# Optimization experiments

Hardware: AMD Instinct MI355X
Metric: run time of the kernel (lower is better)

Reference implementation:

```python
import jax, jax.numpy as jnp
import numpy as np

GRID_SIZE = 5
K = 3  # spline order
WIDTH = [512, 1024, 1024, 1024, 256]
BATCH = 4096


def make_grid(in_dim):
    # pykan-style extended uniform grid on [-1, 1]: G + 2K + 1 knots per input dim
    h = 2.0 / GRID_SIZE
    pts = jnp.arange(-K, GRID_SIZE + K + 1, dtype=jnp.float32) * h - 1.0
    return jnp.tile(pts[None, :], (in_dim, 1))


def bspline_basis(x, grid):
    # Cox-de Boor recursion. x: [B, in], grid: [in, G+2K+1] -> basis [B, in, G+K]
    xe = x[..., None]
    b = ((xe >= grid[:, :-1]) & (xe < grid[:, 1:])).astype(x.dtype)  # degree 0: [B, in, G+2K]
    for d in range(1, K + 1):
        left = (xe - grid[:, :-(d + 1)]) / (grid[:, d:-1] - grid[:, :-(d + 1)]) * b[..., :-1]
        right = (grid[:, d + 1:] - xe) / (grid[:, d + 1:] - grid[:, 1:-d]) * b[..., 1:]
        b = left + right
    return b


def kan_layer(x, grid, coef, scale_base, scale_sp):
    # out_j = sum_i scale_base[i,j]*silu(x_i) + scale_sp[i,j]*sum_g coef[i,j,g]*B_g(x_i)
    basis = bspline_basis(x, grid)                                   # [B, in, G+K]
    base = jnp.einsum('bi,io->bo', jax.nn.silu(x), scale_base)
    spline = jnp.einsum('big,iog->bo', basis, coef * scale_sp[:, :, None])
    return base + spline


def setup_inputs() -> dict:
    key = jax.random.key(0)
    n_layers = len(WIDTH) - 1
    keys = jax.random.split(key, 2 + 2 * n_layers)
    inp = {
        'inputs_y': jax.random.normal(keys[0], (BATCH, 256), dtype=jnp.float32) * 0.5,
        'inputs_u': jax.random.normal(keys[1], (BATCH, 256), dtype=jnp.float32) * 0.5,
    }
    for l, (din, dout) in enumerate(zip(WIDTH[:-1], WIDTH[1:])):
        inp[f'coef{l}'] = jax.random.normal(keys[2 + 2 * l], (din, dout, GRID_SIZE + K), dtype=jnp.float32) * (0.1 / np.sqrt(din))
        inp[f'sb{l}'] = jax.random.normal(keys[3 + 2 * l], (din, dout), dtype=jnp.float32) * (1.0 / np.sqrt(din))
        inp[f'ss{l}'] = jnp.ones((din, dout), dtype=jnp.float32)
        inp[f'grid{l}'] = make_grid(din)
    return inp


def reference(inputs_y, inputs_u,
              coef0, sb0, ss0, grid0,
              coef1, sb1, ss1, grid1,
              coef2, sb2, ss2, grid2,
              coef3, sb3, ss3, grid3):
    x = jnp.concatenate([inputs_y.astype(jnp.float32), inputs_u.astype(jnp.float32)], axis=-1)
    layers = [(grid0, coef0, sb0, ss0), (grid1, coef1, sb1, ss1),
              (grid2, coef2, sb2, ss2), (grid3, coef3, sb3, ss3)]
    for g, c, sb, ss in layers:
        x = kan_layer(x, g, c, sb, ss)
    return x
```

## Files before the change

kernel.cpp:

```cpp
#include <hip/hip_runtime.h>
#include <cstdint>
#include <cstddef>

typedef _Float16 f16;
typedef _Float16 f16x2 __attribute__((ext_vector_type(2)));
typedef _Float16 f16x4 __attribute__((ext_vector_type(4)));
typedef _Float16 f16x8 __attribute__((ext_vector_type(8)));
typedef float f32x4 __attribute__((ext_vector_type(4)));

__device__ __forceinline__ void gl2lds16(const void* g, void* l) {
  __builtin_amdgcn_global_load_lds(
      (const __attribute__((address_space(1))) void*)(uintptr_t)g,
      (__attribute__((address_space(3))) void*)(uintptr_t)l,
      16, 0, 0);
}

__device__ __forceinline__ void kan_basis(float x, f16* out9) {
  float sig  = 1.0f / (1.0f + __expf(-x));
  out9[0] = (f16)(x * sig);

  float t[12];
#pragma unroll
  for (int j = 0; j < 12; ++j) t[j] = (float)(j - 3) * 0.4f - 1.0f;
  float b0[11];
#pragma unroll
  for (int j = 0; j < 11; ++j)
    b0[j] = (x >= t[j] && x < t[j + 1]) ? 1.0f : 0.0f;
  float b1[10];
#pragma unroll
  for (int j = 0; j < 10; ++j)
    b1[j] = (x - t[j]) * 2.5f * b0[j] + (t[j + 2] - x) * 2.5f * b0[j + 1];
  float b2[9];
#pragma unroll
  for (int j = 0; j < 9; ++j)
    b2[j] = (x - t[j]) * 1.25f * b1[j] + (t[j + 3] - x) * 1.25f * b1[j + 1];
#pragma unroll
  for (int j = 0; j < 8; ++j)
    out9[1 + j] = (f16)((x - t[j]) * (1.0f / 1.2f) * b2[j] +
                        (t[j + 4] - x) * (1.0f / 1.2f) * b2[j + 1]);
}

__global__ __launch_bounds__(256) void kan_prep_feat(
    const float* __restrict__ coef, const float* __restrict__ sb,
    const float* __restrict__ ss, f16* __restrict__ Wt,
    const float* __restrict__ Xa, const float* __restrict__ Xb,
    f16* __restrict__ F,
    int dout, int din, int prepBlocks, int featB, int segW, int bShift)
{
  __shared__ float s_sb[32][32];
  __shared__ float s_ss[32][32];
  __shared__ f16 s_w[32][288];
  const int t = threadIdx.x;
  const int gid = blockIdx.x;
  const int K9 = 9 * din;

  if (gid < prepBlocks) {
    const int prepBX = dout >> 5;
    const int o0 = (gid % prepBX) * 32, i0 = (gid / prepBX) * 32;

    {
      int il = t >> 3, oc = (t & 7) * 4;
      float4 vb = *(const float4*)(sb + (size_t)(i0 + il) * dout + o0 + oc);
      float4 vs = *(const float4*)(ss + (size_t)(i0 + il) * dout + o0 + oc);
      s_sb[il][oc + 0] = vb.x; s_sb[il][oc + 1] = vb.y;
      s_sb[il][oc + 2] = vb.z; s_sb[il][oc + 3] = vb.w;
      s_ss[il][oc + 0] = vs.x; s_ss[il][oc + 1] = vs.y;
      s_ss[il][oc + 2] = vs.z; s_ss[il][oc + 3] = vs.w;
    }
    __syncthreads();

#pragma unroll
    for (int j = 0; j < 8; ++j) {
      int f  = j * 256 + t;
      int il = f >> 6, c = f & 63;
      int ol = c >> 1, gh = (c & 1) * 4;
      float4 v = *(const float4*)(coef + ((size_t)(i0 + il) * dout + (o0 + ol)) * 8 + gh);
      float ssv = s_ss[il][ol];
      f16* dst = &s_w[ol][il * 9 + 1 + gh];
      dst[0] = (f16)(v.x * ssv); dst[1] = (f16)(v.y * ssv);
      dst[2] = (f16)(v.z * ssv); dst[3] = (f16)(v.w * ssv);
    }
#pragma unroll
    for (int j = 0; j < 4; ++j) {
      int e = j * 256 + t; int il = e >> 5, ol = e & 31;
      s_w[ol][il * 9] = (f16)s_sb[il][ol];
    }
    __syncthreads();

    {
      int o = t >> 3, part = t & 7;
      f16* dstRow = Wt + (size_t)(o0 + o) * K9 + i0 + part * 4;
#pragma unroll
      for (int tp = 0; tp < 9; ++tp) {
        f16x4 v;
#pragma unroll
        for (int j = 0; j < 4; ++j) v[j] = s_w[o][(part * 4 + j) * 9 + tp];
        *(f16x4*)(dstRow + (size_t)tp * din) = v;
      }
    }
    return;
  }

  int f   = gid - prepBlocks;
  int seg = (f >= featB) ? 1 : 0;
  int fi  = f - seg * featB;
  const float* X = seg ? Xb : Xa;
  const int halfW = segW >> 1;
  int idx2 = fi * 256 + t;
  int b  = idx2 >> bShift;
  int ii = idx2 & (halfW - 1);
  int i  = seg * segW + 2 * ii;

  float2 xv = *(const float2*)(X + (size_t)b * segW + 2 * ii);
  f16 s0[9], s1[9];
  kan_basis(xv.x, s0);
  kan_basis(xv.y, s1);

  f16* o = F + (size_t)b * K9 + i;
#pragma unroll
  for (int tp = 0; tp < 9; ++tp) {
    f16x2 v; v[0] = s0[tp]; v[1] = s1[tp];
    *(f16x2*)(o + (size_t)tp * din) = v;
  }
}

template <int SPLITK>
__global__ __launch_bounds__(256, 2) void kan_gemm(
    const f16* __restrict__ A, const f16* __restrict__ Bt,
    float* __restrict__ C, int N, int K)
{
  __shared__ __align__(16) f16 lds[4][8192];
  const int tid   = threadIdx.x;
  const int lane  = tid & 63;
  const int w     = tid >> 6;
  const int waveM = w >> 1, waveN = w & 1;
  const int l16   = lane & 15, quad = lane >> 4;
  const size_t mBase = (size_t)blockIdx.y * 128;
  const size_t nBase = (size_t)blockIdx.x * 128;
  const int kChunk = K / SPLITK;
  const int k0     = blockIdx.z * kChunk;
  const int kSteps = kChunk >> 5;

  const f16* gA[2]; int lA[2];
  const f16* gB[2]; int lB[2];
#pragma unroll
  for (int r = 0; r < 2; ++r) {
    int g = r * 256 + tid, row = g >> 2;
    int cs = (g & 3) ^ ((row >> 1) & 3);
    gA[r] = A + (mBase + row) * (size_t)K + k0 + cs * 8;
    gB[r] = Bt + (nBase + row) * (size_t)K + k0 + cs * 8;
    lA[r] = (r * 256 + (tid & ~63)) * 8;
    lB[r] = 4096 + lA[r];
  }

  f32x4 acc[4][4] = {};

#pragma unroll
  for (int p = 0; p < 3; ++p) {
    f16* b = lds[p];
    int kk = p * 32;
#pragma unroll
    for (int r = 0; r < 2; ++r) {
      gl2lds16(gA[r] + kk, b + lA[r]);
      gl2lds16(gB[r] + kk, b + lB[r]);
    }
  }

  for (int s = 0; s < kSteps; ++s) {
    if (s < kSteps - 2)       asm volatile("s_waitcnt vmcnt(8)" ::: "memory");
    else if (s == kSteps - 2) asm volatile("s_waitcnt vmcnt(4)" ::: "memory");
    else                      asm volatile("s_waitcnt vmcnt(0)" ::: "memory");
    __builtin_amdgcn_s_barrier();

    if (s + 3 < kSteps) {
      int kk = (s + 3) * 32;
      f16* b = lds[(s + 3) & 3];
#pragma unroll
      for (int r = 0; r < 2; ++r) {
        gl2lds16(gA[r] + kk, b + lA[r]);
        gl2lds16(gB[r] + kk, b + lB[r]);
      }
    }

    const f16* buf = lds[s & 3];
    f16x8 af[4], bf[4];
#pragma unroll
    for (int mi = 0; mi < 4; ++mi) {
      int row = waveM * 64 + mi * 16 + l16;
      af[mi] = *(const f16x8*)(buf + row * 32 + (quad ^ ((row >> 1) & 3)) * 8);
    }
#pragma unroll
    for (int ni = 0; ni < 4; ++ni) {
      int col = waveN * 64 + ni * 16 + l16;
      bf[ni] = *(const f16x8*)(buf + 4096 + col * 32 + (quad ^ ((col >> 1) & 3)) * 8);
    }
#pragma unroll
    for (int mi = 0; mi < 4; ++mi)
#pragma unroll
      for (int ni = 0; ni < 4; ++ni)
        acc[mi][ni] = __builtin_amdgcn_mfma_f32_16x16x32_f16(
            af[mi], bf[ni], acc[mi][ni], 0, 0, 0);
  }

#pragma unroll
  for (int mi = 0; mi < 4; ++mi) {
    size_t row = mBase + waveM * 64 + mi * 16 + quad * 4;
#pragma unroll
    for (int ni = 0; ni < 4; ++ni) {
      size_t col = nBase + waveN * 64 + ni * 16 + l16;
#pragma unroll
      for (int r = 0; r < 4; ++r)
        unsafeAtomicAdd(C + (row + r) * N + col, acc[mi][ni][r]);
    }
  }
}

extern "C" void kernel_launch(void* const* d_in, const int* in_sizes, int n_in,
                              void* d_out, int out_size, void* d_ws, size_t ws_size,
                              hipStream_t stream)
{
  const float* y = (const float*)d_in[0];
  const float* u = (const float*)d_in[1];
  const float* coef[4]; const float* sb[4]; const float* ss[4];
  for (int l = 0; l < 4; ++l) {
    coef[l] = (const float*)d_in[2 + 4 * l];
    sb[l]   = (const float*)d_in[3 + 4 * l];
    ss[l]   = (const float*)d_in[4 + 4 * l];
  }
  char* ws = (char*)d_ws;
  f16*   Wt   = (f16*)(ws);
  f16*   F    = (f16*)(ws + 18874368);
  float* actA = (float*)(ws + 18874368 + 75497472);
  float* actB = (float*)(ws + 18874368 + 75497472 + 16777216);
  float* out  = (float*)d_out;
  const size_t actBytes = (size_t)4096 * 1024 * 4;

  hipMemsetAsync(actA, 0, 2 * actBytes, stream);
  hipMemsetAsync(d_out, 0, (size_t)out_size * sizeof(float), stream);

  kan_prep_feat<<<512 + 4096, 256, 0, stream>>>(
      coef[0], sb[0], ss[0], Wt, y, u, F, 1024, 512, 512, 2048, 256, 7);
  kan_gemm<2><<<dim3(8, 32, 2), 256, 0, stream>>>(F, Wt, actA, 1024, 4608);

  kan_prep_feat<<<1024 + 8192, 256, 0, stream>>>(
      coef[1], sb[1], ss[1], Wt, actA, nullptr, F, 1024, 1024, 1024, 8192, 1024, 9);
  kan_gemm<2><<<dim3(8, 32, 2), 256, 0, stream>>>(F, Wt, actB, 1024, 9216);

  hipMemsetAsync(actA, 0, actBytes, stream);

  kan_prep_feat<<<1024 + 8192, 256, 0, stream>>>(
      coef[2], sb[2], ss[2], Wt, actB, nullptr, F, 1024, 1024, 1024, 8192, 1024, 9);
  kan_gemm<2><<<dim3(8, 32, 2), 256, 0, stream>>>(F, Wt, actA, 1024, 9216);

  kan_prep_feat<<<256 + 8192, 256, 0, stream>>>(
      coef[3], sb[3], ss[3], Wt, actA, nullptr, F, 256, 1024, 256, 8192, 1024, 9);
  kan_gemm<8><<<dim3(2, 32, 8), 256, 0, stream>>>(F, Wt, out, 256, 9216);
}
```

Before: 590.9 us.

## Restructure GEMM pipeline into paired-stage double buffering and drop a memset

The GEMM main loop now processes two 32-wide k-steps per iteration from one half of the 4-slot LDS ring while prefetching the next pair into the other half. This halves the number of barriers but waits for all outstanding loads (vmcnt(0)) each iteration, which reduces prefetch depth compared with the previous three-ahead pipeline. LDS fragment offsets are hoisted out of the loop. When the workspace is large enough, a third activation buffer is used so the mid-sequence memset can be merged into the initial one.

```diff
diff --git a/kernel.cpp b/kernel.cpp
--- a/kernel.cpp
+++ b/kernel.cpp
@@ -153,10 +153,19 @@
     lB[r] = 4096 + lA[r];
   }
 
+  int aOff[4], bOff[4];
+#pragma unroll
+  for (int mi = 0; mi < 4; ++mi) {
+    int row = waveM * 64 + mi * 16 + l16;
+    aOff[mi] = row * 32 + (quad ^ ((row >> 1) & 3)) * 8;
+    int col = waveN * 64 + mi * 16 + l16;
+    bOff[mi] = 4096 + col * 32 + (quad ^ ((col >> 1) & 3)) * 8;
+  }
+
   f32x4 acc[4][4] = {};
 
 #pragma unroll
-  for (int p = 0; p < 3; ++p) {
+  for (int p = 0; p < 2; ++p) {
     f16* b = lds[p];
     int kk = p * 32;
 #pragma unroll
@@ -166,40 +175,41 @@
     }
   }
 
-  for (int s = 0; s < kSteps; ++s) {
-    if (s < kSteps - 2)       asm volatile("s_waitcnt vmcnt(8)" ::: "memory");
-    else if (s == kSteps - 2) asm volatile("s_waitcnt vmcnt(4)" ::: "memory");
-    else                      asm volatile("s_waitcnt vmcnt(0)" ::: "memory");
+  const int nw = kSteps >> 1;
+  for (int wd = 0; wd < nw; ++wd) {
+    asm volatile("s_waitcnt vmcnt(0)" ::: "memory");
     __builtin_amdgcn_s_barrier();
 
-    if (s + 3 < kSteps) {
-      int kk = (s + 3) * 32;
-      f16* b = lds[(s + 3) & 3];
-#pragma unroll
-      for (int r = 0; r < 2; ++r) {
-        gl2lds16(gA[r] + kk, b + lA[r]);
-        gl2lds16(gB[r] + kk, b + lB[r]);
+    const int sp = (wd & 1) * 2;
+    if (2 * wd + 2 < kSteps) {
+      const int spN = ((wd + 1) & 1) * 2;
+#pragma unroll
+      for (int q = 0; q < 2; ++q) {
+        f16* b = lds[spN + q];
+        int kk = (2 * wd + 2 + q) * 32;
+#pragma unroll
+        for (int r = 0; r < 2; ++r) {
+          gl2lds16(gA[r] + kk, b + lA[r]);
+          gl2lds16(gB[r] + kk, b + lB[r]);
+        }
       }
     }
 
-    const f16* buf = lds[s & 3];
-    f16x8 af[4], bf[4];
-#pragma unroll
-    for (int mi = 0; mi < 4; ++mi) {
-      int row = waveM * 64 + mi * 16 + l16;
-      af[mi] = *(const f16x8*)(buf + row * 32 + (quad ^ ((row >> 1) & 3)) * 8);
-    }
-#pragma unroll
-    for (int ni = 0; ni < 4; ++ni) {
-      int col = waveN * 64 + ni * 16 + l16;
-      bf[ni] = *(const f16x8*)(buf + 4096 + col * 32 + (quad ^ ((col >> 1) & 3)) * 8);
-    }
-#pragma unroll
-    for (int mi = 0; mi < 4; ++mi)
-#pragma unroll
-      for (int ni = 0; ni < 4; ++ni)
-        acc[mi][ni] = __builtin_amdgcn_mfma_f32_16x16x32_f16(
-            af[mi], bf[ni], acc[mi][ni], 0, 0, 0);
+#pragma unroll
+    for (int q = 0; q < 2; ++q) {
+      const f16* buf = lds[sp + q];
+      f16x8 af[4], bf[4];
+#pragma unroll
+      for (int mi = 0; mi < 4; ++mi) af[mi] = *(const f16x8*)(buf + aOff[mi]);
+#pragma unroll
+      for (int ni = 0; ni < 4; ++ni) bf[ni] = *(const f16x8*)(buf + bOff[ni]);
+#pragma unroll
+      for (int mi = 0; mi < 4; ++mi)
+#pragma unroll
+        for (int ni = 0; ni < 4; ++ni)
+          acc[mi][ni] = __builtin_amdgcn_mfma_f32_16x16x32_f16(
+              af[mi], bf[ni], acc[mi][ni], 0, 0, 0);
+    }
   }
 
 #pragma unroll
@@ -234,8 +244,11 @@
   float* actB = (float*)(ws + 18874368 + 75497472 + 16777216);
   float* out  = (float*)d_out;
   const size_t actBytes = (size_t)4096 * 1024 * 4;
-
-  hipMemsetAsync(actA, 0, 2 * actBytes, stream);
+  const size_t need3 = 18874368 + 75497472 + 3 * actBytes;
+  const bool  three  = (ws_size >= need3);
+  float* actC = three ? (float*)((char*)actB + actBytes) : actA;
+
+  hipMemsetAsync(actA, 0, (three ? 3 : 2) * actBytes, stream);
   hipMemsetAsync(d_out, 0, (size_t)out_size * sizeof(float), stream);
 
   kan_prep_feat<<<512 + 4096, 256, 0, stream>>>(
@@ -246,13 +259,13 @@
       coef[1], sb[1], ss[1], Wt, actA, nullptr, F, 1024, 1024, 1024, 8192, 1024, 9);
   kan_gemm<2><<<dim3(8, 32, 2), 256, 0, stream>>>(F, Wt, actB, 1024, 9216);
 
-  hipMemsetAsync(actA, 0, actBytes, stream);
+  if (!three) hipMemsetAsync(actA, 0, actBytes, stream);
 
   kan_prep_feat<<<1024 + 8192, 256, 0, stream>>>(
       coef[2], sb[2], ss[2], Wt, actB, nullptr, F, 1024, 1024, 1024, 8192, 1024, 9);
-  kan_gemm<2><<<dim3(8, 32, 2), 256, 0, stream>>>(F, Wt, actA, 1024, 9216);
+  kan_gemm<2><<<dim3(8, 32, 2), 256, 0, stream>>>(F, Wt, actC, 1024, 9216);
 
   kan_prep_feat<<<256 + 8192, 256, 0, stream>>>(
-      coef[3], sb[3], ss[3], Wt, actA, nullptr, F, 256, 1024, 256, 8192, 1024, 9);
+      coef[3], sb[3], ss[3], Wt, actC, nullptr, F, 256, 1024, 256, 8192, 1024, 9);
   kan_gemm<8><<<dim3(2, 32, 8), 256, 0, stream>>>(F, Wt, out, 256, 9216);
 }
```

Measured after the change: 553.5 us. -6.3%, faster.
